# Optimization experiments

Hardware: AMD Instinct MI355X
Metric: run time of the kernel (lower is better)

Reference implementation:

```python
import jax, jax.numpy as jnp
import numpy as np

N, E, G = 10000, 40000, 128          # nodes, edges, graphs
NF, EF, H, NH, GD, L = 92, 50, 64, 10, 108, 5  # feat dims, hidden, heads, global dim, layers
EPS = 1e-5

def _lrelu(v):
    return jax.nn.leaky_relu(v, 0.2)

def setup_inputs() -> dict:
    key = jax.random.key(0)
    ks = jax.random.split(key, 24)
    def rn(k, shp, s=0.05):
        return jax.random.normal(k, shp, jnp.float32) * s
    return {
        "x": jax.random.normal(ks[0], (N, NF), jnp.float32),
        "edge_index": jax.random.randint(ks[1], (2, E), 0, N, dtype=jnp.int32),
        "edge_attr": jax.random.normal(ks[2], (E, EF), jnp.float32),
        "batch_idx": jnp.sort(jax.random.randint(ks[3], (N,), 0, G, dtype=jnp.int32)),
        "global_features": jax.random.normal(ks[4], (G, GD), jnp.float32),
        "node_W": rn(ks[5], (NF, H)), "node_b": jnp.zeros((H,), jnp.float32),
        "edge_W": rn(ks[6], (EF, H)), "edge_b": jnp.zeros((H,), jnp.float32),
        "conv_W": rn(ks[7], (L, 2 * H, NH * H)),
        "conv_att": rn(ks[8], (L, NH, 2 * H)),
        "conv_b": jnp.zeros((L, H), jnp.float32),
        "conv_gamma": jnp.ones((L, NH), jnp.float32),
        "conv_beta": jnp.zeros((L, NH), jnp.float32),
        "ga_W1": rn(ks[9], (H + GD, H)), "ga_b1": jnp.zeros((H,), jnp.float32),
        "ga_W2": rn(ks[10], (H, 1)), "ga_b2": jnp.zeros((1,), jnp.float32),
        "out_W1": rn(ks[11], (H, H)), "out_b1": jnp.zeros((H,), jnp.float32),
        "out_W2": rn(ks[12], (H, 1)), "out_b2": jnp.zeros((1,), jnp.float32),
    }

def reference(x, edge_index, edge_attr, batch_idx, global_features,
              node_W, node_b, edge_W, edge_b,
              conv_W, conv_att, conv_b, conv_gamma, conv_beta,
              ga_W1, ga_b1, ga_W2, ga_b2, out_W1, out_b1, out_W2, out_b2):
    row, col = edge_index[0], edge_index[1]
    # embeddings
    h = _lrelu(x @ node_W + node_b)            # [N, H]
    ea = _lrelu(edge_attr @ edge_W + edge_b)   # [E, H]
    initial = h
    inv_std = 1.0 / jnp.sqrt(1.0 + EPS)        # DiffGroupNorm eval: running mean=0, var=1
    for i in range(L):
        xi = jnp.concatenate([h[row], ea], axis=-1)               # [E, 2H]
        xj = jnp.concatenate([h[col], ea], axis=-1)
        hi = _lrelu(xi @ conv_W[i]).reshape(E, NH, H)             # [E, NH, H]
        hj = _lrelu(xj @ conv_W[i]).reshape(E, NH, H)
        alpha = jnp.sum(jnp.concatenate([hi, hj], -1) * conv_att[i][None], -1)  # [E, NH]
        alpha = _lrelu(alpha)
        alpha = alpha * inv_std * conv_gamma[i] + conv_beta[i]
        alpha = jax.nn.softmax(alpha, axis=1)                     # softmax over heads
        msg = (hj * alpha[..., None]).reshape(E, NH * H)
        agg = jax.ops.segment_sum(msg, row, num_segments=N).reshape(N, NH, H)
        h_new = agg.mean(axis=1) + conv_b[i]
        h = h + h_new if i > 0 else h_new
    h = h + initial
    # global attention: softmax over nodes within each graph
    g = global_features[batch_idx]                                 # [N, GD]
    s = _lrelu(jnp.concatenate([h, g], -1) @ ga_W1 + ga_b1)
    score = (s @ ga_W2 + ga_b2)[:, 0]                              # [N]
    smax = jax.ops.segment_max(score, batch_idx, num_segments=G)
    ex = jnp.exp(score - smax[batch_idx])
    denom = jax.ops.segment_sum(ex, batch_idx, num_segments=G)
    w = (ex / denom[batch_idx])[:, None]
    h = h * w
    pooled = jax.ops.segment_sum(h, batch_idx, num_segments=G)     # [G, H]
    out = jax.nn.relu(pooled @ out_W1 + out_b1) @ out_W2 + out_b2
    return out[:, 0]
```

## Files before the change

### kernel.cpp

```cpp
#include <hip/hip_runtime.h>

#define LRELU(v) ((v) > 0.f ? (v) : 0.2f * (v))

template <int CTRL, int RMASK>
__device__ __forceinline__ float dpp_add(float v) {
  int moved = __builtin_amdgcn_update_dpp(0, __builtin_bit_cast(int, v), CTRL,
                                          RMASK, 0xf, true);
  return v + __builtin_bit_cast(float, moved);
}
__device__ __forceinline__ float wave_sum(float v) {
  v = dpp_add<0x111, 0xf>(v);
  v = dpp_add<0x112, 0xf>(v);
  v = dpp_add<0x114, 0xf>(v);
  v = dpp_add<0x118, 0xf>(v);
  v = dpp_add<0x142, 0xa>(v);
  v = dpp_add<0x143, 0xc>(v);
  return __builtin_bit_cast(
      float, __builtin_amdgcn_readlane(__builtin_bit_cast(int, v), 63));
}

__global__ __launch_bounds__(256) void embed2_kernel(
    const float* __restrict__ x, const float* __restrict__ nW,
    const float* __restrict__ nb, float* __restrict__ h0, int N_,
    const float* __restrict__ eattr, const float* __restrict__ eW,
    const float* __restrict__ eb, float* __restrict__ ea, int E_,
    int nodeBlocks) {
  const int lane = threadIdx.x & 63;
  const float *X, *W, *b;
  float* out;
  int M, K, r;
  if ((int)blockIdx.x < nodeBlocks) {
    r = blockIdx.x * 4 + (threadIdx.x >> 6);
    X = x; W = nW; b = nb; out = h0; M = N_; K = 92;
  } else {
    r = (blockIdx.x - nodeBlocks) * 4 + (threadIdx.x >> 6);
    X = eattr; W = eW; b = eb; out = ea; M = E_; K = 50;
  }
  r = __builtin_amdgcn_readfirstlane(r);
  if (r >= M) return;
  float acc = b[lane];
  const float* Xr = X + (size_t)r * K;
  const float* Wl = W + lane;
  for (int k = 0; k < K; ++k) acc = fmaf(Xr[k], Wl[(size_t)k * 64], acc);
  acc = LRELU(acc);
  out[(size_t)r * 64 + lane] = acc;
}

__global__ __launch_bounds__(256) void count_kernel(const int* __restrict__ row,
                                                    int* __restrict__ cnt,
                                                    int E_) {
  int e = blockIdx.x * 256 + threadIdx.x;
  if (e < E_) atomicAdd(&cnt[row[e]], 1);
}

__global__ __launch_bounds__(256) void scan_kernel(const int* __restrict__ cnt,
                                                   int* __restrict__ cursor,
                                                   int N_) {
  __shared__ int part[256];
  int t = threadIdx.x;
  int per = (N_ + 255) / 256;
  int lo = t * per, hi = min(N_, lo + per);
  int s = 0;
  for (int i = lo; i < hi; ++i) s += cnt[i];
  part[t] = s;
  __syncthreads();
  for (int off = 1; off < 256; off <<= 1) {
    int v = (t >= off) ? part[t - off] : 0;
    __syncthreads();
    part[t] += v;
    __syncthreads();
  }
  int excl = (t == 0) ? 0 : part[t - 1];
  for (int i = lo; i < hi; ++i) {
    cursor[i] = excl;
    excl += cnt[i];
  }
}

__global__ __launch_bounds__(256) void scatter_kernel(
    const int* __restrict__ row, const int* __restrict__ col,
    int* __restrict__ cursor, int* __restrict__ rs, int* __restrict__ cs,
    int* __restrict__ es, int E_) {
  int e = blockIdx.x * 256 + threadIdx.x;
  if (e >= E_) return;
  int r = row[e];
  int p = atomicAdd(&cursor[r], 1);
  rs[p] = r;
  cs[p] = col[e];
  es[p] = e;
}

__global__ __launch_bounds__(256) void gather_ea_kernel(
    const float* __restrict__ ea, const int* __restrict__ es,
    float* __restrict__ eas, int E_) {
  int idx = blockIdx.x * 256 + threadIdx.x;
  if (idx >= E_ * 64) return;
  int p = idx >> 6, c = idx & 63;
  eas[idx] = ea[(size_t)es[p] * 64 + c];
}

__global__ __launch_bounds__(256, 4) void update_gemm_kernel(
    const float* __restrict__ A0, float* __restrict__ h,
    float* __restrict__ agg, const float* __restrict__ bvec,
    const float* __restrict__ W, float* __restrict__ P, int M, int mode) {
  const int lane = threadIdx.x & 63;
  const int wv =
      __builtin_amdgcn_readfirstlane(blockIdx.x * 4 + (threadIdx.x >> 6));
  const int r0 = wv * 4;
  if (r0 >= M) return;
  float hv[4];
  if (mode < 0) {
#pragma unroll
    for (int r = 0; r < 4; ++r) hv[r] = A0[(size_t)(r0 + r) * 64 + lane];
  } else {
    float bl = bvec[lane];
#pragma unroll
    for (int r = 0; r < 4; ++r) {
      size_t idx = (size_t)(r0 + r) * 64 + lane;
      float v = fmaf(agg[idx], 0.1f, bl);
      if (mode >= 1) v += h[idx];
      agg[idx] = 0.f;
      h[idx] = v;
      hv[r] = v;
    }
  }
  float acc[4][10];
#pragma unroll
  for (int r = 0; r < 4; ++r)
#pragma unroll
    for (int q = 0; q < 10; ++q) acc[r][q] = 0.f;
  const float* Wl = W + lane;
  float wa[10], wb[10];
#pragma unroll
  for (int q = 0; q < 10; ++q) wa[q] = Wl[q * 64];
#pragma unroll 1
  for (int k = 0; k < 64; k += 2) {
#pragma unroll
    for (int q = 0; q < 10; ++q) wb[q] = Wl[(k + 1) * 640 + q * 64];
#pragma unroll
    for (int r = 0; r < 4; ++r) {
      float a = __shfl(hv[r], k);
#pragma unroll
      for (int q = 0; q < 10; ++q) acc[r][q] = fmaf(a, wa[q], acc[r][q]);
    }
    if (k + 2 < 64) {
#pragma unroll
      for (int q = 0; q < 10; ++q) wa[q] = Wl[(k + 2) * 640 + q * 64];
    }
#pragma unroll
    for (int r = 0; r < 4; ++r) {
      float a = __shfl(hv[r], k + 1);
#pragma unroll
      for (int q = 0; q < 10; ++q) acc[r][q] = fmaf(a, wb[q], acc[r][q]);
    }
  }
#pragma unroll
  for (int r = 0; r < 4; ++r) {
    float* Crow = P + (size_t)(r0 + r) * 640;
#pragma unroll
    for (int q = 0; q < 10; ++q) Crow[q * 64 + lane] = acc[r][q];
  }
}

__global__ __launch_bounds__(256, 3) void edge_fused_kernel(
    const float* __restrict__ P, const float* __restrict__ eas,
    const float* __restrict__ Wbot,
    const int* __restrict__ rs, const int* __restrict__ cs,
    const float* __restrict__ att, const float* __restrict__ gamma,
    const float* __restrict__ beta, float* __restrict__ agg, int E_) {
  const int lane = threadIdx.x & 63;
  const int wv =
      __builtin_amdgcn_readfirstlane(blockIdx.x * 4 + (threadIdx.x >> 6));
  const int e0 = wv * 8;
  if (e0 >= E_) return;

  int ris[8], cis[8];
#pragma unroll
  for (int r = 0; r < 8; ++r) {
    int e = (e0 + r < E_) ? (e0 + r) : (E_ - 1);
    ris[r] = rs[e];
    cis[r] = cs[e];
  }

  float qacc[8][10];
#pragma unroll
  for (int r = 0; r < 8; ++r)
#pragma unroll
    for (int q = 0; q < 10; ++q) qacc[r][q] = 0.f;

  const float* eaw = eas + (size_t)e0 * 64;
  const float* Wl = Wbot + lane;
  float wa[10], wb[10];
#pragma unroll
  for (int q = 0; q < 10; ++q) wa[q] = Wl[q * 64];
#pragma unroll 1
  for (int k = 0; k < 64; k += 2) {
#pragma unroll
    for (int q = 0; q < 10; ++q) wb[q] = Wl[(k + 1) * 640 + q * 64];
#pragma unroll
    for (int r = 0; r < 8; ++r) {
      float a = eaw[r * 64 + k];
#pragma unroll
      for (int q = 0; q < 10; ++q) qacc[r][q] = fmaf(a, wa[q], qacc[r][q]);
    }
    if (k + 2 < 64) {
#pragma unroll
      for (int q = 0; q < 10; ++q) wa[q] = Wl[(k + 2) * 640 + q * 64];
    }
#pragma unroll
    for (int r = 0; r < 8; ++r) {
      float a = eaw[r * 64 + k + 1];
#pragma unroll
      for (int q = 0; q < 10; ++q) qacc[r][q] = fmaf(a, wb[q], qacc[r][q]);
    }
  }

  const float inv_std = 0.9999950000374997f;
  float gm[10], bt[10];
#pragma unroll
  for (int q = 0; q < 10; ++q) {
    gm[q] = gamma[q];
    bt[q] = beta[q];
  }

  float prb[10], pcb[10];
  {
    const float* Pr = P + (size_t)ris[0] * 640 + lane;
    const float* Pc = P + (size_t)cis[0] * 640 + lane;
#pragma unroll
    for (int q = 0; q < 10; ++q) {
      prb[q] = Pr[q * 64];
      pcb[q] = Pc[q * 64];
    }
  }

  float pend = 0.f;
  int prow = ris[0];

#pragma unroll
  for (int r = 0; r < 8; ++r) {
    if (e0 + r >= E_) break;
    float pr[10], pc[10];
#pragma unroll
    for (int q = 0; q < 10; ++q) {
      pr[q] = prb[q];
      pc[q] = pcb[q];
    }
    if (r + 1 < 8) {
      const float* Pr = P + (size_t)ris[r + 1] * 640 + lane;
      const float* Pc = P + (size_t)cis[r + 1] * 640 + lane;
#pragma unroll
      for (int q = 0; q < 10; ++q) {
        prb[q] = Pr[q * 64];
        pcb[q] = Pc[q * 64];
      }
    }
    float hj[10], sv[10];
#pragma unroll
    for (int q = 0; q < 10; ++q) {
      float qc = qacc[r][q];
      float hi = pr[q] + qc;
      float hjv = pc[q] + qc;
      hi = LRELU(hi);
      hjv = LRELU(hjv);
      hj[q] = hjv;
      float part =
          fmaf(hi, att[q * 128 + lane], hjv * att[q * 128 + 64 + lane]);
      sv[q] = wave_sum(part);
    }
    float mx = -1e30f;
#pragma unroll
    for (int q = 0; q < 10; ++q) {
      float a = sv[q];
      a = LRELU(a);
      a = fmaf(a * inv_std, gm[q], bt[q]);
      sv[q] = a;
      mx = fmaxf(mx, a);
    }
    float ssum = 0.f;
#pragma unroll
    for (int q = 0; q < 10; ++q) {
      float ex = __expf(sv[q] - mx);
      sv[q] = ex;
      ssum += ex;
    }
    float inv = 1.0f / ssum;
    float m = 0.f;
#pragma unroll
    for (int q = 0; q < 10; ++q) m = fmaf(sv[q] * inv, hj[q], m);
    if (ris[r] != prow) {
      atomicAdd(agg + (size_t)prow * 64 + lane, pend);
      pend = 0.f;
      prow = ris[r];
    }
    pend += m;
  }
  atomicAdd(agg + (size_t)prow * 64 + lane, pend);
}

__global__ __launch_bounds__(256) void finalize_kernel(
    float* __restrict__ h, float* __restrict__ agg, const float* __restrict__ b,
    const float* __restrict__ h0, int total) {
  int idx = blockIdx.x * 256 + threadIdx.x;
  if (idx >= total) return;
  int f = idx & 63;
  float v = fmaf(agg[idx], 0.1f, b[f]);
  agg[idx] = 0.f;
  h[idx] = v + h[idx] + h0[idx];
}

__global__ __launch_bounds__(256) void score_kernel(
    const float* __restrict__ h, const int* __restrict__ batch,
    const float* __restrict__ gf, const float* __restrict__ W1,
    const float* __restrict__ b1, const float* __restrict__ W2,
    const float* __restrict__ b2, float* __restrict__ score, int N_) {
  const int lane = threadIdx.x & 63;
  const int n =
      __builtin_amdgcn_readfirstlane(blockIdx.x * 4 + (threadIdx.x >> 6));
  if (n >= N_) return;
  float acc = b1[lane];
  const float* hn = h + (size_t)n * 64;
  const float* W1l = W1 + lane;
#pragma unroll 8
  for (int k = 0; k < 64; ++k) acc = fmaf(hn[k], W1l[k * 64], acc);
  const int bn = batch[n];
  const float* g = gf + (size_t)bn * 108;
#pragma unroll 4
  for (int k = 0; k < 108; ++k) acc = fmaf(g[k], W1l[(64 + k) * 64], acc);
  acc = LRELU(acc);
  float v = wave_sum(acc * W2[lane]);
  if (lane == 0) score[n] = v + b2[0];
}

__global__ void bounds_kernel(const int* __restrict__ batch,
                              int* __restrict__ start, int N_, int G_) {
  int n = blockIdx.x * blockDim.x + threadIdx.x;
  if (n >= N_) return;
  int b = batch[n];
  int bp = (n == 0) ? -1 : batch[n - 1];
  for (int g = bp + 1; g <= b; ++g) start[g] = n;
  if (n == N_ - 1)
    for (int g = b + 1; g <= G_; ++g) start[g] = N_;
}

__global__ __launch_bounds__(256) void pool_out_kernel(
    const float* __restrict__ h, const float* __restrict__ score,
    const int* __restrict__ start, const float* __restrict__ W1,
    const float* __restrict__ b1, const float* __restrict__ W2,
    const float* __restrict__ b2, float* __restrict__ out) {
  int g = blockIdx.x;
  int s0 = start[g], s1 = start[g + 1];
  int tid = threadIdx.x;
  __shared__ float red[256];
  __shared__ float pool[64];
  __shared__ float sh_smax, sh_denom;
  float lm = -1e30f;
  for (int n = s0 + tid; n < s1; n += 256) lm = fmaxf(lm, score[n]);
  red[tid] = lm;
  __syncthreads();
  for (int off = 128; off; off >>= 1) {
    if (tid < off) red[tid] = fmaxf(red[tid], red[tid + off]);
    __syncthreads();
  }
  if (tid == 0) sh_smax = red[0];
  __syncthreads();
  float smax = sh_smax;
  __syncthreads();
  float ls = 0.f;
  for (int n = s0 + tid; n < s1; n += 256) ls += __expf(score[n] - smax);
  red[tid] = ls;
  __syncthreads();
  for (int off = 128; off; off >>= 1) {
    if (tid < off) red[tid] += red[tid + off];
    __syncthreads();
  }
  if (tid == 0) sh_denom = red[0];
  __syncthreads();
  float denom = sh_denom;
  float invd = denom > 0.f ? 1.0f / denom : 0.f;
  __syncthreads();
  int f = tid & 63, sub = tid >> 6;
  float acc = 0.f;
  for (int n = s0 + sub; n < s1; n += 4)
    acc = fmaf(__expf(score[n] - smax), h[(size_t)n * 64 + f], acc);
  red[tid] = acc;
  __syncthreads();
  if (tid < 64)
    pool[tid] =
        (red[tid] + red[tid + 64] + red[tid + 128] + red[tid + 192]) * invd;
  __syncthreads();
  if (tid < 64) {
    float a = b1[tid];
#pragma unroll 8
    for (int k = 0; k < 64; ++k) a = fmaf(pool[k], W1[k * 64 + tid], a);
    a = fmaxf(a, 0.f);
    red[tid] = a * W2[tid];
  }
  __syncthreads();
  if (tid == 0) {
    float s = 0.f;
    for (int k = 0; k < 64; ++k) s += red[k];
    out[g] = s + b2[0];
  }
}

extern "C" void kernel_launch(void* const* d_in, const int* in_sizes, int n_in,
                              void* d_out, int out_size, void* d_ws,
                              size_t ws_size, hipStream_t stream) {
  const float* x          = (const float*)d_in[0];
  const int*   edge_index = (const int*)d_in[1];
  const float* edge_attr  = (const float*)d_in[2];
  const int*   batch_idx  = (const int*)d_in[3];
  const float* gf         = (const float*)d_in[4];
  const float* node_W     = (const float*)d_in[5];
  const float* node_b     = (const float*)d_in[6];
  const float* edge_W     = (const float*)d_in[7];
  const float* edge_b     = (const float*)d_in[8];
  const float* conv_W     = (const float*)d_in[9];
  const float* conv_att   = (const float*)d_in[10];
  const float* conv_b     = (const float*)d_in[11];
  const float* conv_gamma = (const float*)d_in[12];
  const float* conv_beta  = (const float*)d_in[13];
  const float* ga_W1      = (const float*)d_in[14];
  const float* ga_b1      = (const float*)d_in[15];
  const float* ga_W2      = (const float*)d_in[16];
  const float* ga_b2      = (const float*)d_in[17];
  const float* out_W1     = (const float*)d_in[18];
  const float* out_b1     = (const float*)d_in[19];
  const float* out_W2     = (const float*)d_in[20];
  const float* out_b2     = (const float*)d_in[21];
  float* out = (float*)d_out;

  const int N = in_sizes[3];
  const int E = in_sizes[2] / 50;
  const int G = in_sizes[4] / 108;
  const int L = 5;

  float* ws = (float*)d_ws;
  float* h    = ws;  ws += (size_t)N * 64;
  float* h0   = ws;  ws += (size_t)N * 64;
  float* ea   = ws;  ws += (size_t)E * 64;
  float* eas  = ws;  ws += (size_t)E * 64;
  float* P    = ws;  ws += (size_t)N * 640;
  float* agg  = ws;  ws += (size_t)N * 64;
  float* scr  = ws;  ws += N;
  int* gstart = (int*)ws;  ws += G + 8;
  int* cnt    = (int*)ws;  ws += N;
  int* cursor = (int*)ws;  ws += N;
  int* rs     = (int*)ws;  ws += E;
  int* cs     = (int*)ws;  ws += E;
  int* es     = (int*)ws;  ws += E;

  const int* row = edge_index;
  const int* col = edge_index + E;

  int nodeBlocks = (N + 3) / 4;
  int edgeBlocks = (E + 3) / 4;
  embed2_kernel<<<nodeBlocks + edgeBlocks, 256, 0, stream>>>(
      x, node_W, node_b, h0, N, edge_attr, edge_W, edge_b, ea, E, nodeBlocks);

  (void)hipMemsetAsync(cnt, 0, (size_t)N * sizeof(int), stream);
  count_kernel<<<(E + 255) / 256, 256, 0, stream>>>(row, cnt, E);
  scan_kernel<<<1, 256, 0, stream>>>(cnt, cursor, N);
  scatter_kernel<<<(E + 255) / 256, 256, 0, stream>>>(row, col, cursor, rs, cs,
                                                      es, E);
  gather_ea_kernel<<<(E * 64 + 255) / 256, 256, 0, stream>>>(ea, es, eas, E);
  (void)hipMemsetAsync(agg, 0, (size_t)N * 64 * sizeof(float), stream);

  for (int i = 0; i < L; ++i) {
    const float* Wi = conv_W + (size_t)i * 128 * 640;
    if (i == 0) {
      update_gemm_kernel<<<(N / 4 + 3) / 4, 256, 0, stream>>>(
          h0, h, agg, nullptr, Wi, P, N, -1);
    } else {
      update_gemm_kernel<<<(N / 4 + 3) / 4, 256, 0, stream>>>(
          nullptr, h, agg, conv_b + (i - 1) * 64, Wi, P, N,
          (i - 1) == 0 ? 0 : 1);
    }
    int waves = (E + 7) / 8;
    edge_fused_kernel<<<(waves + 3) / 4, 256, 0, stream>>>(
        P, eas, Wi + 64 * 640, rs, cs, conv_att + (size_t)i * 1280,
        conv_gamma + i * 10, conv_beta + i * 10, agg, E);
  }
  finalize_kernel<<<(N * 64 + 255) / 256, 256, 0, stream>>>(
      h, agg, conv_b + (L - 1) * 64, h0, N * 64);

  score_kernel<<<(N + 3) / 4, 256, 0, stream>>>(h, batch_idx, gf, ga_W1, ga_b1,
                                                ga_W2, ga_b2, scr, N);
  bounds_kernel<<<(N + 255) / 256, 256, 0, stream>>>(batch_idx, gstart, N, G);
  pool_out_kernel<<<G, 256, 0, stream>>>(h, scr, gstart, out_W1, out_b1, out_W2,
                                         out_b2, out);
}
```

Measured before the change: 728.4 us.

## Stage GEMM weight tiles in shared memory for update and edge kernels

Both the node update GEMM and the fused edge kernel now cooperatively copy 16-row chunks of the weight matrix into LDS with float4 loads and block barriers. Each wave then reads its weights from LDS instead of global/L1, replacing the old register double-buffered global prefetch. Out-of-range waves no longer exit early, because they must take part in the barriers. Their stores are masked instead. The edge kernel's occupancy hint goes from 3 to 4 blocks, while the new 40KB of LDS per block may itself cap occupancy. The extra barriers also add sync cost.

Result: slower. 789.8 us (+8.4%).

```diff
diff --git a/kernel.cpp b/kernel.cpp
--- a/kernel.cpp
+++ b/kernel.cpp
@@ -103,24 +103,30 @@
     const float* __restrict__ A0, float* __restrict__ h,
     float* __restrict__ agg, const float* __restrict__ bvec,
     const float* __restrict__ W, float* __restrict__ P, int M, int mode) {
-  const int lane = threadIdx.x & 63;
+  __shared__ float Ws[16 * 640];
+  const int tid = threadIdx.x;
+  const int lane = tid & 63;
   const int wv =
-      __builtin_amdgcn_readfirstlane(blockIdx.x * 4 + (threadIdx.x >> 6));
+      __builtin_amdgcn_readfirstlane(blockIdx.x * 4 + (tid >> 6));
   const int r0 = wv * 4;
-  if (r0 >= M) return;
+  const bool active = r0 < M;
+  const int r0c = active ? r0 : 0;
+
   float hv[4];
   if (mode < 0) {
 #pragma unroll
-    for (int r = 0; r < 4; ++r) hv[r] = A0[(size_t)(r0 + r) * 64 + lane];
+    for (int r = 0; r < 4; ++r) hv[r] = A0[(size_t)(r0c + r) * 64 + lane];
   } else {
     float bl = bvec[lane];
 #pragma unroll
     for (int r = 0; r < 4; ++r) {
-      size_t idx = (size_t)(r0 + r) * 64 + lane;
+      size_t idx = (size_t)(r0c + r) * 64 + lane;
       float v = fmaf(agg[idx], 0.1f, bl);
       if (mode >= 1) v += h[idx];
-      agg[idx] = 0.f;
-      h[idx] = v;
+      if (active) {
+        agg[idx] = 0.f;
+        h[idx] = v;
+      }
       hv[r] = v;
     }
   }
@@ -129,55 +135,58 @@
   for (int r = 0; r < 4; ++r)
 #pragma unroll
     for (int q = 0; q < 10; ++q) acc[r][q] = 0.f;
-  const float* Wl = W + lane;
-  float wa[10], wb[10];
-#pragma unroll
-  for (int q = 0; q < 10; ++q) wa[q] = Wl[q * 64];
+
 #pragma unroll 1
-  for (int k = 0; k < 64; k += 2) {
-#pragma unroll
-    for (int q = 0; q < 10; ++q) wb[q] = Wl[(k + 1) * 640 + q * 64];
+  for (int c = 0; c < 4; ++c) {
+    __syncthreads();
+    const float4* src = (const float4*)(W + (size_t)c * 16 * 640);
+    float4* dst = (float4*)Ws;
+#pragma unroll
+    for (int j = 0; j < 10; ++j) dst[j * 256 + tid] = src[j * 256 + tid];
+    __syncthreads();
+#pragma unroll 1
+    for (int kk = 0; kk < 16; ++kk) {
+      int k = c * 16 + kk;
+      float w[10];
+#pragma unroll
+      for (int q = 0; q < 10; ++q) w[q] = Ws[kk * 640 + q * 64 + lane];
+#pragma unroll
+      for (int r = 0; r < 4; ++r) {
+        float a = __shfl(hv[r], k);
+#pragma unroll
+        for (int q = 0; q < 10; ++q) acc[r][q] = fmaf(a, w[q], acc[r][q]);
+      }
+    }
+  }
+  if (active) {
 #pragma unroll
     for (int r = 0; r < 4; ++r) {
-      float a = __shfl(hv[r], k);
-#pragma unroll
-      for (int q = 0; q < 10; ++q) acc[r][q] = fmaf(a, wa[q], acc[r][q]);
-    }
-    if (k + 2 < 64) {
-#pragma unroll
-      for (int q = 0; q < 10; ++q) wa[q] = Wl[(k + 2) * 640 + q * 64];
-    }
-#pragma unroll
-    for (int r = 0; r < 4; ++r) {
-      float a = __shfl(hv[r], k + 1);
-#pragma unroll
-      for (int q = 0; q < 10; ++q) acc[r][q] = fmaf(a, wb[q], acc[r][q]);
-    }
-  }
-#pragma unroll
-  for (int r = 0; r < 4; ++r) {
-    float* Crow = P + (size_t)(r0 + r) * 640;
-#pragma unroll
-    for (int q = 0; q < 10; ++q) Crow[q * 64 + lane] = acc[r][q];
-  }
-}
-
-__global__ __launch_bounds__(256, 3) void edge_fused_kernel(
+      float* Crow = P + (size_t)(r0 + r) * 640;
+#pragma unroll
+      for (int q = 0; q < 10; ++q) Crow[q * 64 + lane] = acc[r][q];
+    }
+  }
+}
+
+__global__ __launch_bounds__(256, 4) void edge_fused_kernel(
     const float* __restrict__ P, const float* __restrict__ eas,
     const float* __restrict__ Wbot,
     const int* __restrict__ rs, const int* __restrict__ cs,
     const float* __restrict__ att, const float* __restrict__ gamma,
     const float* __restrict__ beta, float* __restrict__ agg, int E_) {
-  const int lane = threadIdx.x & 63;
+  __shared__ float Ws[16 * 640];
+  const int tid = threadIdx.x;
+  const int lane = tid & 63;
   const int wv =
-      __builtin_amdgcn_readfirstlane(blockIdx.x * 4 + (threadIdx.x >> 6));
+      __builtin_amdgcn_readfirstlane(blockIdx.x * 4 + (tid >> 6));
   const int e0 = wv * 8;
-  if (e0 >= E_) return;
+  const bool active = e0 < E_;
+  const int e0c = active ? e0 : 0;
 
   int ris[8], cis[8];
 #pragma unroll
   for (int r = 0; r < 8; ++r) {
-    int e = (e0 + r < E_) ? (e0 + r) : (E_ - 1);
+    int e = (e0c + r < E_) ? (e0c + r) : (E_ - 1);
     ris[r] = rs[e];
     cis[r] = cs[e];
   }
@@ -188,32 +197,32 @@
 #pragma unroll
     for (int q = 0; q < 10; ++q) qacc[r][q] = 0.f;
 
-  const float* eaw = eas + (size_t)e0 * 64;
-  const float* Wl = Wbot + lane;
-  float wa[10], wb[10];
-#pragma unroll
-  for (int q = 0; q < 10; ++q) wa[q] = Wl[q * 64];
+  const float* eaw = eas + (size_t)e0c * 64;
+
 #pragma unroll 1
-  for (int k = 0; k < 64; k += 2) {
-#pragma unroll
-    for (int q = 0; q < 10; ++q) wb[q] = Wl[(k + 1) * 640 + q * 64];
-#pragma unroll
-    for (int r = 0; r < 8; ++r) {
-      float a = eaw[r * 64 + k];
-#pragma unroll
-      for (int q = 0; q < 10; ++q) qacc[r][q] = fmaf(a, wa[q], qacc[r][q]);
-    }
-    if (k + 2 < 64) {
-#pragma unroll
-      for (int q = 0; q < 10; ++q) wa[q] = Wl[(k + 2) * 640 + q * 64];
-    }
-#pragma unroll
-    for (int r = 0; r < 8; ++r) {
-      float a = eaw[r * 64 + k + 1];
-#pragma unroll
-      for (int q = 0; q < 10; ++q) qacc[r][q] = fmaf(a, wb[q], qacc[r][q]);
-    }
-  }
+  for (int c = 0; c < 4; ++c) {
+    __syncthreads();
+    const float4* src = (const float4*)(Wbot + (size_t)c * 16 * 640);
+    float4* dst = (float4*)Ws;
+#pragma unroll
+    for (int j = 0; j < 10; ++j) dst[j * 256 + tid] = src[j * 256 + tid];
+    __syncthreads();
+#pragma unroll 1
+    for (int kk = 0; kk < 16; ++kk) {
+      int k = c * 16 + kk;
+      float w[10];
+#pragma unroll
+      for (int q = 0; q < 10; ++q) w[q] = Ws[kk * 640 + q * 64 + lane];
+#pragma unroll
+      for (int r = 0; r < 8; ++r) {
+        float a = eaw[r * 64 + k];
+#pragma unroll
+        for (int q = 0; q < 10; ++q) qacc[r][q] = fmaf(a, w[q], qacc[r][q]);
+      }
+    }
+  }
+
+  if (!active) return;
 
   const float inv_std = 0.9999950000374997f;
   float gm[10], bt[10];
```
